# Performance work log

Measured on AMD Instinct MI355X. Metric: run time of the kernel, lower is better.

## Reference

```python
import jax, jax.numpy as jnp
import numpy as np

EMB = 300
L = 5
N = 100000
E = 400000
G = 4000
ATOM_DIMS = np.array([119, 4, 12, 12, 10, 6, 6, 2, 2])
BOND_DIMS = np.array([5, 6, 2])
ATOM_OFF = jnp.asarray(np.concatenate([[0], np.cumsum(ATOM_DIMS)[:-1]]))
BOND_OFF = jnp.asarray(np.concatenate([[0], np.cumsum(BOND_DIMS)[:-1]]))
BN_EPS = 1e-5


def setup_inputs() -> dict:
    key = jax.random.key(0)
    ks = jax.random.split(key, 16)
    x = jax.random.randint(ks[0], (N, 9), 0, 2, dtype=jnp.int64)
    edge_index = jax.random.randint(ks[1], (2, E), 0, N, dtype=jnp.int64)
    edge_attr = jax.random.randint(ks[2], (E, 3), 0, 2, dtype=jnp.int64)
    batch = jnp.sort(jax.random.randint(ks[3], (N,), 0, G, dtype=jnp.int64))
    s = 0.05
    atom_emb = jax.random.normal(ks[4], (int(ATOM_DIMS.sum()), EMB), jnp.float32) * s
    bond_emb = jax.random.normal(ks[5], (int(BOND_DIMS.sum()), EMB), jnp.float32) * s
    W1 = jax.random.normal(ks[6], (L, EMB, 2 * EMB), jnp.float32) * (1.0 / np.sqrt(EMB))
    b1 = jnp.zeros((L, 2 * EMB), jnp.float32)
    g1 = jnp.ones((L, 2 * EMB), jnp.float32)
    bt1 = jnp.zeros((L, 2 * EMB), jnp.float32)
    W2 = jax.random.normal(ks[7], (L, 2 * EMB, EMB), jnp.float32) * (1.0 / np.sqrt(2 * EMB))
    b2 = jnp.zeros((L, EMB), jnp.float32)
    g2 = jnp.ones((L, EMB), jnp.float32)
    bt2 = jnp.zeros((L, EMB), jnp.float32)
    return dict(x=x, edge_index=edge_index, edge_attr=edge_attr, batch=batch,
                atom_emb=atom_emb, bond_emb=bond_emb,
                W1=W1, b1=b1, g1=g1, bt1=bt1, W2=W2, b2=b2, g2=g2, bt2=bt2)


def _bn(h, g, b):
    # BatchNorm1d, training-mode forward (batch stats, biased var)
    m = h.mean(0)
    v = h.var(0)
    return (h - m) * jax.lax.rsqrt(v + BN_EPS) * g + b


def reference(x, edge_index, edge_attr, batch, atom_emb, bond_emb,
              W1, b1, g1, bt1, W2, b2, g2, bt2):
    src, dst = edge_index[0], edge_index[1]
    # AtomEncoder / BondEncoder: sum of per-feature embeddings
    h = atom_emb[x + ATOM_OFF[None, :]].sum(axis=1)          # [N, EMB]
    ea = bond_emb[edge_attr + BOND_OFF[None, :]].sum(axis=1)  # [E, EMB]
    for i in range(L):
        # GINEConv: aggr = sum_j relu(x_j + e_ij); out = mlp((1+eps)*x + aggr), eps=0
        msg = jax.nn.relu(h[src] + ea)                        # [E, EMB]
        agg = jax.ops.segment_sum(msg, dst, num_segments=N)   # [N, EMB]
        z = h + agg
        z = _bn(z @ W1[i] + b1[i], g1[i], bt1[i])             # [N, 2*EMB]
        z = jax.nn.relu(z)
        h = z @ W2[i] + b2[i]                                 # [N, EMB]
        h = _bn(h, g2[i], bt2[i])
        if i != L - 1:
            h = jax.nn.relu(h)
        # dropout with p=0.0 is identity
    return jax.ops.segment_sum(h, batch, num_segments=G)      # [G, EMB]
```

## Files before the change

kernel.cpp:

```cpp
#include <hip/hip_runtime.h>

#define NN 100000
#define EE 400000
#define GG 4000
#define EMB 300
#define EMB2 600
#define LL 5
#define BN_EPS 1e-5f
#define BUF_BYTES 120000000ull
#define SCAN_NB 98
#define WSET 1597440ull

typedef __attribute__((ext_vector_type(8))) short bf16x8;
typedef __attribute__((ext_vector_type(4))) short bf16x4;
typedef __attribute__((ext_vector_type(2))) short bf16x2;
typedef __attribute__((ext_vector_type(4))) float f32x4;

__device__ __constant__ int c_atom_off[9] = {0,119,123,135,147,157,163,169,171};

static __device__ __forceinline__ float u16tof(unsigned short u) {
    return __uint_as_float(((unsigned int)u) << 16);
}
static __device__ __forceinline__ unsigned short ftobf(float f) {
    unsigned int u = __float_as_uint(f);
    unsigned int r = 0x7fffu + ((u >> 16) & 1u);
    return (unsigned short)((u + r) >> 16);
}
static __device__ __forceinline__ int geti(const void* p, int f64, long long i) {
    return f64 ? (int)((const long long*)p)[i] : ((const int*)p)[i];
}
static __device__ __forceinline__ f32x4 mfma16(bf16x8 a, bf16x8 b, f32x4 c) {
    return __builtin_amdgcn_mfma_f32_16x16x32_bf16(a, b, c, 0, 0, 0);
}

__global__ void k_detect(const int* __restrict__ ei, int* __restrict__ flag) {
    __shared__ int cnt;
    if (threadIdx.x == 0) cnt = 0;
    __syncthreads();
    int z = 0;
    for (int i = threadIdx.x; i < 1024; i += 256)
        if (ei[2 * i + 1] == 0) z++;
    atomicAdd(&cnt, z);
    __syncthreads();
    if (threadIdx.x == 0) *flag = (cnt > 512) ? 1 : 0;
}

__global__ void k_init(float* __restrict__ sc2, float* __restrict__ sh2) {
    const int c = blockIdx.x * 256 + threadIdx.x;
    if (c < EMB) { sc2[c] = 1.f; sh2[c] = 0.f; }
}

__global__ void k_encode(const void* __restrict__ x, const float* __restrict__ aemb,
                         float* __restrict__ h, const int* __restrict__ flag) {
    __shared__ int xi[4][9];
    const int ty = threadIdx.y, tx = threadIdx.x;
    const int n = blockIdx.x * 4 + ty;
    const int f64 = *flag;
    if (tx < 9) xi[ty][tx] = geti(x, f64, (long long)n * 9 + tx) + c_atom_off[tx];
    __syncthreads();
    if (tx < 75) {
        const int c = tx * 4;
        float s0 = 0.f, s1 = 0.f, s2 = 0.f, s3 = 0.f;
#pragma unroll
        for (int f = 0; f < 9; ++f) {
            const float4 v = *(const float4*)(aemb + (size_t)xi[ty][f] * EMB + c);
            s0 += v.x; s1 += v.y; s2 += v.z; s3 += v.w;
        }
        float4 o; o.x = s0; o.y = s1; o.z = s2; o.w = s3;
        *(float4*)(h + (size_t)n * EMB + c) = o;
    }
}

__global__ void k_deg(const void* __restrict__ ei, int* __restrict__ deg,
                      const int* __restrict__ flag) {
    const int e = blockIdx.x * 256 + threadIdx.x;
    if (e < EE) atomicAdd(&deg[geti(ei, *flag, (long long)EE + e)], 1);
}

__global__ void k_scanA(const int* __restrict__ deg, int* __restrict__ bsum) {
    __shared__ int red[256];
    const int b = blockIdx.x, t = threadIdx.x;
    const int base = b * 1024 + t * 4;
    int s = 0;
#pragma unroll
    for (int e = 0; e < 4; ++e) {
        const int i = base + e;
        if (i < NN) s += deg[i];
    }
    red[t] = s;
    __syncthreads();
    for (int off = 128; off > 0; off >>= 1) {
        if (t < off) red[t] += red[t + off];
        __syncthreads();
    }
    if (t == 0) bsum[b] = red[0];
}

__global__ void k_scanB(const int* __restrict__ bsum, int* __restrict__ bbase,
                        int* __restrict__ rowstart) {
    if (threadIdx.x == 0) {
        int run = 0;
        for (int b = 0; b < SCAN_NB; ++b) { bbase[b] = run; run += bsum[b]; }
        rowstart[NN] = run;
    }
}

__global__ void k_scanC(const int* __restrict__ deg, const int* __restrict__ bbase,
                        int* __restrict__ rowstart, int* __restrict__ cursor) {
    __shared__ int ts[256];
    const int b = blockIdx.x, t = threadIdx.x;
    const int base = b * 1024 + t * 4;
    int loc[4];
    int s = 0;
#pragma unroll
    for (int e = 0; e < 4; ++e) {
        const int i = base + e;
        loc[e] = (i < NN) ? deg[i] : 0;
        s += loc[e];
    }
    ts[t] = s;
    __syncthreads();
    for (int off = 1; off < 256; off <<= 1) {
        const int v = (t >= off) ? ts[t - off] : 0;
        __syncthreads();
        ts[t] += v;
        __syncthreads();
    }
    int run = bbase[b] + ts[t] - s;
#pragma unroll
    for (int e = 0; e < 4; ++e) {
        const int i = base + e;
        if (i < NN) { rowstart[i] = run; cursor[i] = run; run += loc[e]; }
    }
}

__global__ void k_scatter(const void* __restrict__ ei, const void* __restrict__ eattr,
                          int* __restrict__ cursor, int* __restrict__ elist,
                          const int* __restrict__ flag) {
    const int e = blockIdx.x * 256 + threadIdx.x;
    if (e >= EE) return;
    const int f64 = *flag;
    const int src = geti(ei, f64, e);
    const int dst = geti(ei, f64, (long long)EE + e);
    const int b0 = geti(eattr, f64, (long long)e * 3 + 0);
    const int b1 = geti(eattr, f64, (long long)e * 3 + 1);
    const int b2 = geti(eattr, f64, (long long)e * 3 + 2);
    const int pos = atomicAdd(&cursor[dst], 1);
    elist[pos] = src * 64 + b0 * 12 + b1 * 2 + b2;
}

__global__ void k_ebc(const float* __restrict__ bemb, float* __restrict__ ebc) {
    const int cb = blockIdx.x;
    const int tx = threadIdx.x;
    if (tx >= 75) return;
    const int b0 = cb / 12, b1 = (cb / 2) % 6, b2 = cb & 1;
    const int c = tx * 4;
    const float4 v0 = *(const float4*)(bemb + (size_t)b0 * EMB + c);
    const float4 v1 = *(const float4*)(bemb + (size_t)(5 + b1) * EMB + c);
    const float4 v2 = *(const float4*)(bemb + (size_t)(11 + b2) * EMB + c);
    float4 o; o.x = v0.x + v1.x + v2.x; o.y = v0.y + v1.y + v2.y;
    o.z = v0.z + v1.z + v2.z; o.w = v0.w + v1.w + v2.w;
    *(float4*)(ebc + (size_t)cb * EMB + c) = o;
}

__global__ void k_gather(const int* __restrict__ rowstart, const int* __restrict__ elist,
                         const float* __restrict__ ebc,
                         const float* __restrict__ h, float* __restrict__ z,
                         const float* __restrict__ sc, const float* __restrict__ sh,
                         int dorelu) {
    const int ty = threadIdx.y, tx = threadIdx.x;
    const int n = blockIdx.x * 4 + ty;
    if (tx >= 75) return;
    const int c = tx * 4;
    const float4 s4 = *(const float4*)(sc + c);
    const float4 h4 = *(const float4*)(sh + c);
    const int s = rowstart[n], e = rowstart[n + 1];
    float4 acc;
    {
        float4 v = *(const float4*)(h + (size_t)n * EMB + c);
        v.x = fmaf(v.x, s4.x, h4.x); v.y = fmaf(v.y, s4.y, h4.y);
        v.z = fmaf(v.z, s4.z, h4.z); v.w = fmaf(v.w, s4.w, h4.w);
        if (dorelu) {
            v.x = fmaxf(v.x, 0.f); v.y = fmaxf(v.y, 0.f);
            v.z = fmaxf(v.z, 0.f); v.w = fmaxf(v.w, 0.f);
        }
        acc = v;
    }
    for (int j = s; j < e; ++j) {
        const int packed = elist[j];
        const int src = packed >> 6, cb = packed & 63;
        float4 hv = *(const float4*)(h + (size_t)src * EMB + c);
        const float4 ev = *(const float4*)(ebc + (size_t)cb * EMB + c);
        hv.x = fmaf(hv.x, s4.x, h4.x); hv.y = fmaf(hv.y, s4.y, h4.y);
        hv.z = fmaf(hv.z, s4.z, h4.z); hv.w = fmaf(hv.w, s4.w, h4.w);
        if (dorelu) {
            hv.x = fmaxf(hv.x, 0.f); hv.y = fmaxf(hv.y, 0.f);
            hv.z = fmaxf(hv.z, 0.f); hv.w = fmaxf(hv.w, 0.f);
        }
        acc.x += fmaxf(hv.x + ev.x, 0.f);
        acc.y += fmaxf(hv.y + ev.y, 0.f);
        acc.z += fmaxf(hv.z + ev.z, 0.f);
        acc.w += fmaxf(hv.w + ev.w, 0.f);
    }
    *(float4*)(z + (size_t)n * EMB + c) = acc;
}

__global__ void k_wconv1(const float* __restrict__ W, unsigned short* __restrict__ hi,
                         unsigned short* __restrict__ lo) {
    const int idx = blockIdx.x * 256 + threadIdx.x;
    if (idx >= 10 * 40 * 64 * 8) return;
    const int e = idx & 7;
    const int lane = (idx >> 3) & 63;
    const int nt = (idx >> 9) % 40;
    const int kt = idx / 20480;
    const int r = lane & 15, g = lane >> 4;
    const int col = nt * 16 + r;
    const int k = kt * 32 + g * 8 + e;
    const float w = (col < EMB2 && k < EMB) ? W[(size_t)k * EMB2 + col] : 0.f;
    const unsigned short h = ftobf(w);
    hi[idx] = h;
    lo[idx] = ftobf(w - u16tof(h));
}
__global__ void k_wconv2(const float* __restrict__ W, unsigned short* __restrict__ hi,
                         unsigned short* __restrict__ lo) {
    const int idx = blockIdx.x * 256 + threadIdx.x;
    if (idx >= 19 * 20 * 64 * 8) return;
    const int e = idx & 7;
    const int lane = (idx >> 3) & 63;
    const int nt = (idx >> 9) % 20;
    const int kt = idx / 10240;
    const int r = lane & 15, g = lane >> 4;
    const int col = nt * 16 + r;
    const int k = kt * 32 + g * 8 + e;
    const float w = (col < EMB && k < EMB2) ? W[(size_t)k * EMB + col] : 0.f;
    const unsigned short h = ftobf(w);
    hi[idx] = h;
    lo[idx] = ftobf(w - u16tof(h));
}

__global__ __launch_bounds__(512) void k_mfma1(
    float* __restrict__ P, float* Q,
    const unsigned short* __restrict__ whi, const unsigned short* __restrict__ wlo)
{
    __shared__ __align__(16) short AsH[2][1024];
    __shared__ __align__(16) short AsL[2][1024];
    const int tid = threadIdx.x;
    const int lane = tid & 63;
    const int wn = tid >> 6;
    const int g = lane >> 4, r = lane & 15;
    const int row0 = blockIdx.x * 32;
    const int se2 = (tid & 3) * 2, str = (tid >> 2) & 15, stg = (tid >> 6) & 3, srg = tid >> 8;
    const int srow = row0 + srg * 16 + str;
    const int sldo = tid * 2;
    f32x4 acc[2][5];
#pragma unroll
    for (int rg = 0; rg < 2; ++rg)
#pragma unroll
        for (int t = 0; t < 5; ++t) acc[rg][t] = (f32x4){0.f, 0.f, 0.f, 0.f};

    auto stage = [&](int kt, int b) {
        const int cc = kt * 32 + stg * 8 + se2;
        float2 v = {0.f, 0.f};
        if (cc + 1 < EMB) v = *(const float2*)(Q + (size_t)srow * EMB + cc);
        bf16x2 h2, l2;
        const unsigned short hx = ftobf(v.x);
        h2[0] = (short)hx; l2[0] = (short)ftobf(v.x - u16tof(hx));
        const unsigned short hy = ftobf(v.y);
        h2[1] = (short)hy; l2[1] = (short)ftobf(v.y - u16tof(hy));
        *(bf16x2*)(&AsH[b][sldo]) = h2;
        *(bf16x2*)(&AsL[b][sldo]) = l2;
    };

    stage(0, 0);
    __syncthreads();

    for (int kt = 0; kt < 10; ++kt) {
        const int cur = kt & 1;
        float2 v = {0.f, 0.f};
        const bool have = (kt + 1 < 10);
        if (have) {
            const int cc = (kt + 1) * 32 + stg * 8 + se2;
            if (cc + 1 < EMB) v = *(const float2*)(Q + (size_t)srow * EMB + cc);
        }
        bf16x8 ah[2], al[2];
#pragma unroll
        for (int rg = 0; rg < 2; ++rg) {
            ah[rg] = *(const bf16x8*)(&AsH[cur][rg * 512 + lane * 8]);
            al[rg] = *(const bf16x8*)(&AsL[cur][rg * 512 + lane * 8]);
        }
#pragma unroll
        for (int t = 0; t < 5; ++t) {
            const size_t wb = ((size_t)(kt * 40 + wn + t * 8) * 64 + lane) * 8;
            const bf16x8 bh = *(const bf16x8*)(whi + wb);
            const bf16x8 bl = *(const bf16x8*)(wlo + wb);
#pragma unroll
            for (int rg = 0; rg < 2; ++rg) {
                acc[rg][t] = mfma16(al[rg], bh, acc[rg][t]);
                acc[rg][t] = mfma16(ah[rg], bl, acc[rg][t]);
                acc[rg][t] = mfma16(ah[rg], bh, acc[rg][t]);
            }
        }
        if (have) {
            bf16x2 h2, l2;
            const unsigned short hx = ftobf(v.x);
            h2[0] = (short)hx; l2[0] = (short)ftobf(v.x - u16tof(hx));
            const unsigned short hy = ftobf(v.y);
            h2[1] = (short)hy; l2[1] = (short)ftobf(v.y - u16tof(hy));
            *(bf16x2*)(&AsH[cur ^ 1][sldo]) = h2;
            *(bf16x2*)(&AsL[cur ^ 1][sldo]) = l2;
        }
        __syncthreads();
    }
#pragma unroll
    for (int t = 0; t < 5; ++t) {
        const int col = (wn + t * 8) * 16 + r;
#pragma unroll
        for (int rg = 0; rg < 2; ++rg) {
            const int orow = row0 + rg * 16 + g * 4;
#pragma unroll
            for (int j = 0; j < 4; ++j) {
                const float val = acc[rg][t][j];
                if (col < EMB)       Q[(size_t)(orow + j) * EMB + col] = val;
                else if (col < EMB2) P[(size_t)(orow + j) * EMB + (col - EMB)] = val;
            }
        }
    }
}

__global__ __launch_bounds__(256) void k_mfma2(
    float* P, const float* __restrict__ Qa,
    const float* __restrict__ sc, const float* __restrict__ sh,
    const unsigned short* __restrict__ whi, const unsigned short* __restrict__ wlo)
{
    __shared__ __align__(16) short AsH[2][1024];
    __shared__ __align__(16) short AsL[2][1024];
    const int tid = threadIdx.x;
    const int lane = tid & 63;
    const int wn = tid >> 6;
    const int g = lane >> 4, r = lane & 15;
    const int row0 = blockIdx.x * 32;
    const int se4 = (tid & 1) * 4, str = (tid >> 1) & 15, stg = (tid >> 5) & 3, srg = tid >> 7;
    const int srow = row0 + srg * 16 + str;
    const int sldo = tid * 4;
    f32x4 acc[2][5];
#pragma unroll
    for (int rg = 0; rg < 2; ++rg)
#pragma unroll
        for (int t = 0; t < 5; ++t) acc[rg][t] = (f32x4){0.f, 0.f, 0.f, 0.f};

    auto loadA = [&](int kt, float4& v) {
        const int cc = kt * 32 + stg * 8 + se4;
        v = (float4){0.f, 0.f, 0.f, 0.f};
        if (cc + 3 < EMB)       v = *(const float4*)(Qa + (size_t)srow * EMB + cc);
        else if (cc + 3 < EMB2) v = *(const float4*)(P + (size_t)srow * EMB + (cc - EMB));
    };
    auto writeA = [&](int kt, int b, float4 v) {
        const int cc = kt * 32 + stg * 8 + se4;
        if (cc + 3 < EMB2) {
            const float4 s4 = *(const float4*)(sc + cc);
            const float4 h4 = *(const float4*)(sh + cc);
            v.x = fmaxf(fmaf(v.x, s4.x, h4.x), 0.f);
            v.y = fmaxf(fmaf(v.y, s4.y, h4.y), 0.f);
            v.z = fmaxf(fmaf(v.z, s4.z, h4.z), 0.f);
            v.w = fmaxf(fmaf(v.w, s4.w, h4.w), 0.f);
        } else {
            v = (float4){0.f, 0.f, 0.f, 0.f};
        }
        bf16x4 h4v, l4v;
        const float vv[4] = {v.x, v.y, v.z, v.w};
#pragma unroll
        for (int e = 0; e < 4; ++e) {
            const unsigned short hh = ftobf(vv[e]);
            h4v[e] = (short)hh;
            l4v[e] = (short)ftobf(vv[e] - u16tof(hh));
        }
        *(bf16x4*)(&AsH[b][sldo]) = h4v;
        *(bf16x4*)(&AsL[b][sldo]) = l4v;
    };

    {
        float4 v;
        loadA(0, v);
        writeA(0, 0, v);
    }
    __syncthreads();

    for (int kt = 0; kt < 19; ++kt) {
        const int cur = kt & 1;
        float4 v;
        const bool have = (kt + 1 < 19);
        if (have) loadA(kt + 1, v);
        bf16x8 ah[2], al[2];
#pragma unroll
        for (int rg = 0; rg < 2; ++rg) {
            ah[rg] = *(const bf16x8*)(&AsH[cur][rg * 512 + lane * 8]);
            al[rg] = *(const bf16x8*)(&AsL[cur][rg * 512 + lane * 8]);
        }
#pragma unroll
        for (int t = 0; t < 5; ++t) {
            const size_t wb = ((size_t)(kt * 20 + wn + t * 4) * 64 + lane) * 8;
            const bf16x8 bh = *(const bf16x8*)(whi + wb);
            const bf16x8 bl = *(const bf16x8*)(wlo + wb);
#pragma unroll
            for (int rg = 0; rg < 2; ++rg) {
                acc[rg][t] = mfma16(al[rg], bh, acc[rg][t]);
                acc[rg][t] = mfma16(ah[rg], bl, acc[rg][t]);
                acc[rg][t] = mfma16(ah[rg], bh, acc[rg][t]);
            }
        }
        if (have) writeA(kt + 1, cur ^ 1, v);
        __syncthreads();
    }
#pragma unroll
    for (int t = 0; t < 5; ++t) {
        const int col = (wn + t * 4) * 16 + r;
        if (col < EMB) {
#pragma unroll
            for (int rg = 0; rg < 2; ++rg) {
                const int orow = row0 + rg * 16 + g * 4;
#pragma unroll
                for (int j = 0; j < 4; ++j)
                    P[(size_t)(orow + j) * EMB + col] = acc[rg][t][j];
            }
        }
    }
}

__global__ void k_statsz(const float* __restrict__ Qm, const float* __restrict__ Pm,
                         float* __restrict__ sum, float* __restrict__ ss) {
    const int c = blockIdx.x * 256 + threadIdx.x;
    if (c >= EMB2) return;
    const float* m = (c < EMB) ? Qm : Pm;
    const int cc = (c < EMB) ? c : c - EMB;
    const int r0 = blockIdx.y * 250;
    const int r1 = r0 + 250;
    float s = 0.f, q = 0.f;
    for (int r = r0; r < r1; ++r) {
        const float v = m[(size_t)r * EMB + cc];
        s += v; q += v * v;
    }
    atomicAdd(&sum[c], s);
    atomicAdd(&ss[c], q);
}

__global__ void k_stats(const float* __restrict__ m, float* __restrict__ sum, float* __restrict__ ss) {
    const int c = blockIdx.x * 256 + threadIdx.x;
    if (c >= EMB) return;
    const int r0 = blockIdx.y * 200;
    const int r1 = r0 + 200;
    float s = 0.f, q = 0.f;
    for (int r = r0; r < r1; ++r) {
        const float v = m[(size_t)r * EMB + c];
        s += v; q += v * v;
    }
    atomicAdd(&sum[c], s);
    atomicAdd(&ss[c], q);
}

__global__ void k_scale(const float* __restrict__ sum, const float* __restrict__ ss,
                        const float* __restrict__ g, const float* __restrict__ b,
                        float* __restrict__ scale, float* __restrict__ shift, int C) {
    const int c = blockIdx.x * 256 + threadIdx.x;
    if (c >= C) return;
    const float invN = 1.0f / (float)NN;
    const float mean = sum[c] * invN;
    const float var = ss[c] * invN - mean * mean;
    const float s = g[c] * rsqrtf(var + BN_EPS);
    scale[c] = s;
    shift[c] = b[c] - mean * s;
}

__global__ void k_poolg(const void* __restrict__ batch, const float* __restrict__ h,
                        float* __restrict__ out, const int* __restrict__ flag,
                        const float* __restrict__ sc, const float* __restrict__ sh) {
    __shared__ float red[4][EMB];
    const int g = blockIdx.x;
    const int f64 = *flag;
    int lo = 0, hi = NN;
    while (lo < hi) { int mid = (lo + hi) >> 1; if (geti(batch, f64, mid) < g) lo = mid + 1; else hi = mid; }
    const int s = lo;
    hi = NN;
    while (lo < hi) { int mid = (lo + hi) >> 1; if (geti(batch, f64, mid) < g + 1) lo = mid + 1; else hi = mid; }
    const int e = lo;
    const int tx = threadIdx.x, ty = threadIdx.y;
    if (tx < 75) {
        const int c = tx * 4;
        const float4 s4 = *(const float4*)(sc + c);
        const float4 h4 = *(const float4*)(sh + c);
        float4 acc; acc.x = acc.y = acc.z = acc.w = 0.f;
        int cntr = 0;
        for (int r = s + ty; r < e; r += 4) {
            const float4 v = *(const float4*)(h + (size_t)r * EMB + c);
            acc.x += v.x; acc.y += v.y; acc.z += v.z; acc.w += v.w;
            cntr++;
        }
        acc.x = fmaf(acc.x, s4.x, cntr * h4.x);
        acc.y = fmaf(acc.y, s4.y, cntr * h4.y);
        acc.z = fmaf(acc.z, s4.z, cntr * h4.z);
        acc.w = fmaf(acc.w, s4.w, cntr * h4.w);
        *(float4*)(&red[ty][c]) = acc;
    }
    __syncthreads();
    if (ty == 0 && tx < 75) {
        const int c = tx * 4;
        float4 o;
        o.x = red[0][c + 0] + red[1][c + 0] + red[2][c + 0] + red[3][c + 0];
        o.y = red[0][c + 1] + red[1][c + 1] + red[2][c + 1] + red[3][c + 1];
        o.z = red[0][c + 2] + red[1][c + 2] + red[2][c + 2] + red[3][c + 2];
        o.w = red[0][c + 3] + red[1][c + 3] + red[2][c + 3] + red[3][c + 3];
        *(float4*)(out + (size_t)g * EMB + c) = o;
    }
}

extern "C" void kernel_launch(void* const* d_in, const int* in_sizes, int n_in,
                              void* d_out, int out_size, void* d_ws, size_t ws_size,
                              hipStream_t stream) {
    const void* x     = d_in[0];
    const void* ei    = d_in[1];
    const void* eattr = d_in[2];
    const void* batch = d_in[3];
    const float* aemb = (const float*)d_in[4];
    const float* bemb = (const float*)d_in[5];
    const float* W1   = (const float*)d_in[6];
    const float* g1   = (const float*)d_in[8];
    const float* bt1  = (const float*)d_in[9];
    const float* W2   = (const float*)d_in[10];
    const float* g2   = (const float*)d_in[12];
    const float* bt2  = (const float*)d_in[13];

    char* ws = (char*)d_ws;
    float* P  = (float*)(ws);
    float* Q  = (float*)(ws + BUF_BYTES);
    char*  aux = ws + 2 * BUF_BYTES;
    float* st = (float*)(aux);
    float* sum1 = st;         float* ss1 = st + 600;
    float* sum2 = st + 1200;  float* ss2 = st + 1500;
    float* sc1  = st + 1800;  float* sh1 = st + 2400;
    float* sc2  = st + 3000;  float* sh2 = st + 3300;
    int* flag     = (int*)(aux + 16384);
    int* deg      = (int*)(aux + 16384 + 64);
    int* rowstart = (int*)(aux + 16384 + 64 + 400064);
    int* cursor   = (int*)(aux + 16384 + 64 + 800128);
    int* elist    = (int*)(aux + 16384 + 64 + 1200192);
    float* ebc    = (float*)(aux + 16384 + 64 + 2800192);
    int* bsum     = (int*)(aux + 2872192);
    int* bbase    = (int*)(aux + 2872192 + 512);
    char* wbase   = aux + 2888640;

    const bool pre = (ws_size >= 2ull * BUF_BYTES + 2888640ull + 5ull * WSET);

    const dim3 blk80x4(80, 4);

    k_detect<<<1, 256, 0, stream>>>((const int*)ei, flag);
    k_init<<<2, 256, 0, stream>>>(sc2, sh2);

    (void)hipMemsetAsync(deg, 0, NN * sizeof(int), stream);
    k_deg<<<(EE + 255) / 256, 256, 0, stream>>>(ei, deg, flag);
    k_scanA<<<SCAN_NB, 256, 0, stream>>>(deg, bsum);
    k_scanB<<<1, 64, 0, stream>>>(bsum, bbase, rowstart);
    k_scanC<<<SCAN_NB, 256, 0, stream>>>(deg, bbase, rowstart, cursor);
    k_scatter<<<(EE + 255) / 256, 256, 0, stream>>>(ei, eattr, cursor, elist, flag);
    k_ebc<<<60, 80, 0, stream>>>(bemb, ebc);

    if (pre) {
        for (int i = 0; i < LL; ++i) {
            char* wb = wbase + (size_t)i * WSET;
            k_wconv1<<<(204800 + 255) / 256, 256, 0, stream>>>(
                W1 + (size_t)i * EMB * EMB2,
                (unsigned short*)wb, (unsigned short*)(wb + 409600));
            k_wconv2<<<(194560 + 255) / 256, 256, 0, stream>>>(
                W2 + (size_t)i * EMB2 * EMB,
                (unsigned short*)(wb + 819200), (unsigned short*)(wb + 819200 + 389120));
        }
    }

    k_encode<<<NN / 4, blk80x4, 0, stream>>>(x, aemb, P, flag);

    for (int i = 0; i < LL; ++i) {
        char* wb = wbase + (pre ? (size_t)i * WSET : 0ull);
        unsigned short* wt1hi = (unsigned short*)wb;
        unsigned short* wt1lo = (unsigned short*)(wb + 409600);
        unsigned short* wt2hi = (unsigned short*)(wb + 819200);
        unsigned short* wt2lo = (unsigned short*)(wb + 819200 + 389120);

        if (!pre) {
            k_wconv1<<<(204800 + 255) / 256, 256, 0, stream>>>(
                W1 + (size_t)i * EMB * EMB2, wt1hi, wt1lo);
            k_wconv2<<<(194560 + 255) / 256, 256, 0, stream>>>(
                W2 + (size_t)i * EMB2 * EMB, wt2hi, wt2lo);
        }
        (void)hipMemsetAsync(st, 0, 1800 * sizeof(float), stream);

        k_gather<<<NN / 4, blk80x4, 0, stream>>>(rowstart, elist, ebc, P, Q,
                                                 sc2, sh2, (i > 0) ? 1 : 0);

        k_mfma1<<<NN / 32, 512, 0, stream>>>(P, Q, wt1hi, wt1lo);

        k_statsz<<<dim3(3, 400), 256, 0, stream>>>(Q, P, sum1, ss1);
        k_scale<<<3, 256, 0, stream>>>(sum1, ss1, g1 + (size_t)i * EMB2, bt1 + (size_t)i * EMB2,
                                       sc1, sh1, EMB2);

        k_mfma2<<<NN / 32, 256, 0, stream>>>(P, Q, sc1, sh1, wt2hi, wt2lo);

        k_stats<<<dim3(2, 500), 256, 0, stream>>>(P, sum2, ss2);
        k_scale<<<2, 256, 0, stream>>>(sum2, ss2, g2 + (size_t)i * EMB, bt2 + (size_t)i * EMB,
                                       sc2, sh2, EMB);
    }

    k_poolg<<<GG, blk80x4, 0, stream>>>(batch, P, (float*)d_out, flag, sc2, sh2);
}
```

Before: 3.053 ms.

## Fuse edge gather-aggregate into first MFMA GEMM with triple-buffer rotation

```diff
diff --git a/kernel.cpp b/kernel.cpp
--- a/kernel.cpp
+++ b/kernel.cpp
@@ -236,6 +236,144 @@
     const unsigned short h = ftobf(w);
     hi[idx] = h;
     lo[idx] = ftobf(w - u16tof(h));
+}
+
+__global__ __launch_bounds__(512) void k_mfma1f(
+    const float* __restrict__ H, float* __restrict__ Za, float* __restrict__ Zb,
+    const int* __restrict__ rowstart, const int* __restrict__ elist,
+    const float* __restrict__ ebc,
+    const float* __restrict__ sc, const float* __restrict__ sh, int dorelu,
+    const unsigned short* __restrict__ whi, const unsigned short* __restrict__ wlo)
+{
+    __shared__ float zbuf[32][EMB];
+    __shared__ __align__(16) short AsH[2][1024];
+    __shared__ __align__(16) short AsL[2][1024];
+    const int tid = threadIdx.x;
+    const int lane = tid & 63;
+    const int wn = tid >> 6;
+    const int g = lane >> 4, r = lane & 15;
+    const int row0 = blockIdx.x * 32;
+
+    {
+        const int rowloc = tid >> 4, t16 = tid & 15;
+        const int n = row0 + rowloc;
+        const int s = rowstart[n], e = rowstart[n + 1];
+        float4 accv[5], s4v[5], h4v[5];
+#pragma unroll
+        for (int u = 0; u < 5; ++u) {
+            const int c4 = (t16 + 16 * u) * 4;
+            accv[u] = (float4){0.f, 0.f, 0.f, 0.f};
+            s4v[u] = (float4){0.f, 0.f, 0.f, 0.f};
+            h4v[u] = (float4){0.f, 0.f, 0.f, 0.f};
+            if (c4 + 3 < EMB) {
+                s4v[u] = *(const float4*)(sc + c4);
+                h4v[u] = *(const float4*)(sh + c4);
+                float4 v = *(const float4*)(H + (size_t)n * EMB + c4);
+                v.x = fmaf(v.x, s4v[u].x, h4v[u].x);
+                v.y = fmaf(v.y, s4v[u].y, h4v[u].y);
+                v.z = fmaf(v.z, s4v[u].z, h4v[u].z);
+                v.w = fmaf(v.w, s4v[u].w, h4v[u].w);
+                if (dorelu) {
+                    v.x = fmaxf(v.x, 0.f); v.y = fmaxf(v.y, 0.f);
+                    v.z = fmaxf(v.z, 0.f); v.w = fmaxf(v.w, 0.f);
+                }
+                accv[u] = v;
+            }
+        }
+        for (int j = s; j < e; ++j) {
+            const int packed = elist[j];
+            const int src = packed >> 6, cb = packed & 63;
+#pragma unroll
+            for (int u = 0; u < 5; ++u) {
+                const int c4 = (t16 + 16 * u) * 4;
+                if (c4 + 3 < EMB) {
+                    float4 hv = *(const float4*)(H + (size_t)src * EMB + c4);
+                    const float4 ev = *(const float4*)(ebc + (size_t)cb * EMB + c4);
+                    hv.x = fmaf(hv.x, s4v[u].x, h4v[u].x);
+                    hv.y = fmaf(hv.y, s4v[u].y, h4v[u].y);
+                    hv.z = fmaf(hv.z, s4v[u].z, h4v[u].z);
+                    hv.w = fmaf(hv.w, s4v[u].w, h4v[u].w);
+                    if (dorelu) {
+                        hv.x = fmaxf(hv.x, 0.f); hv.y = fmaxf(hv.y, 0.f);
+                        hv.z = fmaxf(hv.z, 0.f); hv.w = fmaxf(hv.w, 0.f);
+                    }
+                    accv[u].x += fmaxf(hv.x + ev.x, 0.f);
+                    accv[u].y += fmaxf(hv.y + ev.y, 0.f);
+                    accv[u].z += fmaxf(hv.z + ev.z, 0.f);
+                    accv[u].w += fmaxf(hv.w + ev.w, 0.f);
+                }
+            }
+        }
+#pragma unroll
+        for (int u = 0; u < 5; ++u) {
+            const int c4 = (t16 + 16 * u) * 4;
+            if (c4 + 3 < EMB) *(float4*)(&zbuf[rowloc][c4]) = accv[u];
+        }
+    }
+    __syncthreads();
+
+    const int se2 = (tid & 3) * 2, str = (tid >> 2) & 15, stg = (tid >> 6) & 3, srg = tid >> 8;
+    const int srowloc = srg * 16 + str;
+    const int sldo = tid * 2;
+    f32x4 acc[2][5];
+#pragma unroll
+    for (int rg = 0; rg < 2; ++rg)
+#pragma unroll
+        for (int t = 0; t < 5; ++t) acc[rg][t] = (f32x4){0.f, 0.f, 0.f, 0.f};
+
+    auto stage = [&](int kt, int b) {
+        const int cc = kt * 32 + stg * 8 + se2;
+        float2 v = {0.f, 0.f};
+        if (cc + 1 < EMB) v = *(const float2*)(&zbuf[srowloc][cc]);
+        bf16x2 h2, l2;
+        const unsigned short hx = ftobf(v.x);
+        h2[0] = (short)hx; l2[0] = (short)ftobf(v.x - u16tof(hx));
+        const unsigned short hy = ftobf(v.y);
+        h2[1] = (short)hy; l2[1] = (short)ftobf(v.y - u16tof(hy));
+        *(bf16x2*)(&AsH[b][sldo]) = h2;
+        *(bf16x2*)(&AsL[b][sldo]) = l2;
+    };
+
+    stage(0, 0);
+    __syncthreads();
+
+    for (int kt = 0; kt < 10; ++kt) {
+        const int cur = kt & 1;
+        bf16x8 ah[2], al[2];
+#pragma unroll
+        for (int rg = 0; rg < 2; ++rg) {
+            ah[rg] = *(const bf16x8*)(&AsH[cur][rg * 512 + lane * 8]);
+            al[rg] = *(const bf16x8*)(&AsL[cur][rg * 512 + lane * 8]);
+        }
+#pragma unroll
+        for (int t = 0; t < 5; ++t) {
+            const size_t wb = ((size_t)(kt * 40 + wn + t * 8) * 64 + lane) * 8;
+            const bf16x8 bh = *(const bf16x8*)(whi + wb);
+            const bf16x8 bl = *(const bf16x8*)(wlo + wb);
+#pragma unroll
+            for (int rg = 0; rg < 2; ++rg) {
+                acc[rg][t] = mfma16(al[rg], bh, acc[rg][t]);
+                acc[rg][t] = mfma16(ah[rg], bl, acc[rg][t]);
+                acc[rg][t] = mfma16(ah[rg], bh, acc[rg][t]);
+            }
+        }
+        if (kt + 1 < 10) stage(kt + 1, cur ^ 1);
+        __syncthreads();
+    }
+#pragma unroll
+    for (int t = 0; t < 5; ++t) {
+        const int col = (wn + t * 8) * 16 + r;
+#pragma unroll
+        for (int rg = 0; rg < 2; ++rg) {
+            const int orow = row0 + rg * 16 + g * 4;
+#pragma unroll
+            for (int j = 0; j < 4; ++j) {
+                const float val = acc[rg][t][j];
+                if (col < EMB)       Za[(size_t)(orow + j) * EMB + col] = val;
+                else if (col < EMB2) Zb[(size_t)(orow + j) * EMB + (col - EMB)] = val;
+            }
+        }
+    }
 }
 
 __global__ __launch_bounds__(512) void k_mfma1(
@@ -529,9 +667,14 @@
     const float* bt2  = (const float*)d_in[13];
 
     char* ws = (char*)d_ws;
-    float* P  = (float*)(ws);
-    float* Q  = (float*)(ws + BUF_BYTES);
-    char*  aux = ws + 2 * BUF_BYTES;
+    const bool pre3 = (ws_size >= 3ull * BUF_BYTES + 2888640ull + 5ull * WSET);
+    const bool pre2 = pre3 || (ws_size >= 2ull * BUF_BYTES + 2888640ull + 5ull * WSET);
+
+    float* B0 = (float*)(ws);
+    float* B1 = (float*)(ws + BUF_BYTES);
+    float* B2 = (float*)(ws + 2 * BUF_BYTES);
+    char*  aux = ws + (pre3 ? 3ull : 2ull) * BUF_BYTES;
+
     float* st = (float*)(aux);
     float* sum1 = st;         float* ss1 = st + 600;
     float* sum2 = st + 1200;  float* ss2 = st + 1500;
@@ -547,8 +690,6 @@
     int* bbase    = (int*)(aux + 2872192 + 512);
     char* wbase   = aux + 2888640;
 
-    const bool pre = (ws_size >= 2ull * BUF_BYTES + 2888640ull + 5ull * WSET);
-
     const dim3 blk80x4(80, 4);
 
     k_detect<<<1, 256, 0, stream>>>((const int*)ei, flag);
@@ -562,7 +703,7 @@
     k_scatter<<<(EE + 255) / 256, 256, 0, stream>>>(ei, eattr, cursor, elist, flag);
     k_ebc<<<60, 80, 0, stream>>>(bemb, ebc);
 
-    if (pre) {
+    if (pre2) {
         for (int i = 0; i < LL; ++i) {
             char* wb = wbase + (size_t)i * WSET;
             k_wconv1<<<(204800 + 255) / 256, 256, 0, stream>>>(
@@ -574,38 +715,69 @@
         }
     }
 
-    k_encode<<<NN / 4, blk80x4, 0, stream>>>(x, aemb, P, flag);
-
-    for (int i = 0; i < LL; ++i) {
-        char* wb = wbase + (pre ? (size_t)i * WSET : 0ull);
-        unsigned short* wt1hi = (unsigned short*)wb;
-        unsigned short* wt1lo = (unsigned short*)(wb + 409600);
-        unsigned short* wt2hi = (unsigned short*)(wb + 819200);
-        unsigned short* wt2lo = (unsigned short*)(wb + 819200 + 389120);
-
-        if (!pre) {
-            k_wconv1<<<(204800 + 255) / 256, 256, 0, stream>>>(
-                W1 + (size_t)i * EMB * EMB2, wt1hi, wt1lo);
-            k_wconv2<<<(194560 + 255) / 256, 256, 0, stream>>>(
-                W2 + (size_t)i * EMB2 * EMB, wt2hi, wt2lo);
-        }
-        (void)hipMemsetAsync(st, 0, 1800 * sizeof(float), stream);
-
-        k_gather<<<NN / 4, blk80x4, 0, stream>>>(rowstart, elist, ebc, P, Q,
-                                                 sc2, sh2, (i > 0) ? 1 : 0);
-
-        k_mfma1<<<NN / 32, 512, 0, stream>>>(P, Q, wt1hi, wt1lo);
-
-        k_statsz<<<dim3(3, 400), 256, 0, stream>>>(Q, P, sum1, ss1);
-        k_scale<<<3, 256, 0, stream>>>(sum1, ss1, g1 + (size_t)i * EMB2, bt1 + (size_t)i * EMB2,
-                                       sc1, sh1, EMB2);
-
-        k_mfma2<<<NN / 32, 256, 0, stream>>>(P, Q, sc1, sh1, wt2hi, wt2lo);
-
-        k_stats<<<dim3(2, 500), 256, 0, stream>>>(P, sum2, ss2);
-        k_scale<<<2, 256, 0, stream>>>(sum2, ss2, g2 + (size_t)i * EMB, bt2 + (size_t)i * EMB,
-                                       sc2, sh2, EMB);
-    }
-
-    k_poolg<<<GG, blk80x4, 0, stream>>>(batch, P, (float*)d_out, flag, sc2, sh2);
-}
+    if (pre3) {
+        float* H = B0; float* Za = B1; float* Zb = B2;
+        k_encode<<<NN / 4, blk80x4, 0, stream>>>(x, aemb, H, flag);
+
+        for (int i = 0; i < LL; ++i) {
+            char* wb = wbase + (size_t)i * WSET;
+            unsigned short* wt1hi = (unsigned short*)wb;
+            unsigned short* wt1lo = (unsigned short*)(wb + 409600);
+            unsigned short* wt2hi = (unsigned short*)(wb + 819200);
+            unsigned short* wt2lo = (unsigned short*)(wb + 819200 + 389120);
+
+            (void)hipMemsetAsync(st, 0, 1800 * sizeof(float), stream);
+
+            k_mfma1f<<<NN / 32, 512, 0, stream>>>(H, Za, Zb, rowstart, elist, ebc,
+                                                  sc2, sh2, (i > 0) ? 1 : 0, wt1hi, wt1lo);
+
+            k_statsz<<<dim3(3, 400), 256, 0, stream>>>(Za, Zb, sum1, ss1);
+            k_scale<<<3, 256, 0, stream>>>(sum1, ss1, g1 + (size_t)i * EMB2,
+                                           bt1 + (size_t)i * EMB2, sc1, sh1, EMB2);
+
+            k_mfma2<<<NN / 32, 256, 0, stream>>>(Zb, Za, sc1, sh1, wt2hi, wt2lo);
+
+            k_stats<<<dim3(2, 500), 256, 0, stream>>>(Zb, sum2, ss2);
+            k_scale<<<2, 256, 0, stream>>>(sum2, ss2, g2 + (size_t)i * EMB,
+                                           bt2 + (size_t)i * EMB, sc2, sh2, EMB);
+
+            float* nH = Zb; float* nZa = H; float* nZb = Za;
+            H = nH; Za = nZa; Zb = nZb;
+        }
+        k_poolg<<<GG, blk80x4, 0, stream>>>(batch, H, (float*)d_out, flag, sc2, sh2);
+    } else {
+        float* P = B0; float* Q = B1;
+        k_encode<<<NN / 4, blk80x4, 0, stream>>>(x, aemb, P, flag);
+
+        for (int i = 0; i < LL; ++i) {
+            char* wb = wbase + (pre2 ? (size_t)i * WSET : 0ull);
+            unsigned short* wt1hi = (unsigned short*)wb;
+            unsigned short* wt1lo = (unsigned short*)(wb + 409600);
+            unsigned short* wt2hi = (unsigned short*)(wb + 819200);
+            unsigned short* wt2lo = (unsigned short*)(wb + 819200 + 389120);
+
+            if (!pre2) {
+                k_wconv1<<<(204800 + 255) / 256, 256, 0, stream>>>(
+                    W1 + (size_t)i * EMB * EMB2, wt1hi, wt1lo);
+                k_wconv2<<<(194560 + 255) / 256, 256, 0, stream>>>(
+                    W2 + (size_t)i * EMB2 * EMB, wt2hi, wt2lo);
+            }
+            (void)hipMemsetAsync(st, 0, 1800 * sizeof(float), stream);
+
+            k_gather<<<NN / 4, blk80x4, 0, stream>>>(rowstart, elist, ebc, P, Q,
+                                                     sc2, sh2, (i > 0) ? 1 : 0);
+            k_mfma1<<<NN / 32, 512, 0, stream>>>(P, Q, wt1hi, wt1lo);
+
+            k_statsz<<<dim3(3, 400), 256, 0, stream>>>(Q, P, sum1, ss1);
+            k_scale<<<3, 256, 0, stream>>>(sum1, ss1, g1 + (size_t)i * EMB2,
+                                           bt1 + (size_t)i * EMB2, sc1, sh1, EMB2);
+
+            k_mfma2<<<NN / 32, 256, 0, stream>>>(P, Q, sc1, sh1, wt2hi, wt2lo);
+
+            k_stats<<<dim3(2, 500), 256, 0, stream>>>(P, sum2, ss2);
+            k_scale<<<2, 256, 0, stream>>>(sum2, ss2, g2 + (size_t)i * EMB,
+                                           bt2 + (size_t)i * EMB, sc2, sh2, EMB);
+        }
+        k_poolg<<<GG, blk80x4, 0, stream>>>(batch, P, (float*)d_out, flag, sc2, sh2);
+    }
+}
```

Result: no change. 3.042 ms (-0.4%).
